# Performance work log

Hardware: AMD Instinct MI355X
Metric: run time of the kernel (lower is better)

## Reference

```python
import math
import jax, jax.numpy as jnp
import numpy as np
from jax import lax

jax.config.update("jax_enable_x64", True)

DECOMP_LEVEL = 5
# Daubechies-5 (db5) decomposition low-pass filter (pywt convention)
_DB5_LO = np.array([0.003335725285001549, -0.012580751999015526, -0.006241490213011705,
                    0.07757149384006515, -0.03224486958502952, -0.24229488706619015,
                    0.13842814590110342, 0.7243085284385744, 0.6038292697974729,
                    0.160102397974125], dtype=np.float64)
_L = _DB5_LO.size
_DB5_HI = _DB5_LO[::-1].copy() * ((-1.0) ** np.arange(_L))  # QMF high-pass
LO = jnp.asarray(_DB5_LO, jnp.float32)
HI = jnp.asarray(_DB5_HI, jnp.float32)
LOR = jnp.asarray(_DB5_LO[::-1].copy(), jnp.float32)
HIR = jnp.asarray(_DB5_HI[::-1].copy(), jnp.float32)


def _an_last(x):
    # orthonormal periodized analysis along last axis: (..., n) -> (..., n/2) x2
    n = x.shape[-1]
    lead = x.shape[:-1]
    xp = jnp.concatenate([x, x[..., : _L - 2]], axis=-1).reshape(-1, 1, n + _L - 2)
    k = jnp.stack([LO, HI])[:, None, :]  # (2,1,L)
    y = lax.conv_general_dilated(xp, k, (2,), "VALID")  # (B,2,n/2)
    y = y.reshape(lead + (2, n // 2))
    return y[..., 0, :], y[..., 1, :]


def _syn_last(a, d):
    # exact transpose/inverse of _an_last (orthonormal -> W^T = W^-1)
    n2 = a.shape[-1]
    n = 2 * n2
    lead = a.shape[:-1]
    B = int(np.prod(lead)) if lead else 1
    u = jnp.zeros((B, 2, n), a.dtype)
    u = u.at[:, 0, ::2].set(a.reshape(B, n2))
    u = u.at[:, 1, ::2].set(d.reshape(B, n2))
    up = jnp.concatenate([u[..., -(_L - 1):], u], axis=-1)  # circular left pad
    k = jnp.stack([LOR, HIR])[None, :, :]  # (1,2,L)
    y = lax.conv_general_dilated(up, k, (1,), "VALID")  # (B,1,n)
    return y.reshape(lead + (n,))


def _dwt2(x):  # x: (C,h,w) -> ll, lh, hl, hh each (C,h/2,w/2)
    a_h, d_h = _an_last(x.swapaxes(-1, -2))
    a_h = a_h.swapaxes(-1, -2)
    d_h = d_h.swapaxes(-1, -2)
    ll, lh = _an_last(a_h)
    hl, hh = _an_last(d_h)
    return ll, lh, hl, hh


def _idwt2(ll, lh, hl, hh):
    a_h = _syn_last(ll, lh)
    d_h = _syn_last(hl, hh)
    return _syn_last(a_h.swapaxes(-1, -2), d_h.swapaxes(-1, -2)).swapaxes(-1, -2)


def _estimate_noise(data):
    p = data.shape[0]
    rr = data @ data.T
    rri = jnp.linalg.inv(rr + 1e-6 * jnp.eye(p, dtype=data.dtype))
    def per_band(i):
        xx = rri - jnp.outer(rri[:, i], rri[i, :]) / rri[i, i]
        beta = xx @ rr[:, i]
        return beta.at[i].set(0.0)
    betas = jax.vmap(per_band)(jnp.arange(p))  # (p,p)
    return data - betas @ data


def hyres_forward(x):
    H, W, K = x.shape
    N = H * W
    data = x.reshape(N, K).T.astype(jnp.float64)
    w = _estimate_noise(data)
    omega1 = (jnp.sqrt(jnp.var(w, axis=1, ddof=1)) + 1e-30) ** 2  # (K,) f64
    y_w = x * omega1 ** -0.5  # whitened, f64
    u, s, v_pca = jnp.linalg.svd(y_w.reshape(N, K), full_matrices=False)
    pc = (u * s).reshape(W, H, K).astype(jnp.float32).transpose(2, 0, 1)  # (K,H,W)
    # multi-level 2D DWT per channel
    ll = pc
    highs = []
    for _ in range(DECOMP_LEVEL):
        ll, lh, hl, hh = _dwt2(ll)
        highs.append((lh, hl, hh))
    # overwrite-style full coefficient image [[LL,LH],[HL,HH]] recursively
    full = ll
    for lh, hl, hh in reversed(highs):
        top = jnp.concatenate([full, lh], axis=-1)
        bot = jnp.concatenate([hl, hh], axis=-1)
        full = jnp.concatenate([top, bot], axis=-2)
    V = full.transpose(1, 2, 0).reshape(N, K)
    V2 = V * V
    norm_v = jnp.sum(V2)
    n_xyz = jnp.asarray(V.size, jnp.float32)
    col_norm = jnp.sum(V2, axis=0)  # (K,)
    # SURE of soft-threshold over a 15-point grid in [0, sqrt(log N)]
    ts = np.linspace(0.0, math.sqrt(math.log(N)), 15).astype(np.float32)
    sure_cols = []
    for t in ts:
        t2 = float(t * t)
        s_t = (jnp.sum(jnp.minimum(V2, t2), axis=0)
               + 2.0 * jnp.sum((V2 > t2).astype(jnp.float32), axis=0)
               - col_norm)
        sure_cols.append(s_t)
    sure_all = jnp.stack(sure_cols, axis=1)  # (K,15)
    c_const = norm_v - n_xyz
    # replicate the in-place cumulative update: S_r = sum_{j<r} S_j + sure_r + C
    def step(acc, sure_r):
        s_r = acc + sure_r + c_const
        return acc + s_r, jnp.min(s_r)
    _, min_sure = lax.scan(step, jnp.zeros((15,), jnp.float32), sure_all)
    # early-exit: first rank>1 where min_sure increases; else loop ends at K-1
    cond = min_sure[2:] > min_sure[1:-1]
    rank = jnp.where(jnp.any(cond), 2 + jnp.argmax(cond), K - 1)
    mask = (jnp.arange(K) < rank).astype(jnp.float32)[:, None, None]
    # truncation-to-rank == zeroing channels >= rank (inverse DWT is linear)
    y = ll * mask
    for lh, hl, hh in reversed(highs):
        y = _idwt2(y, lh * mask, hl * mask, hh * mask)
    y_est = y.transpose(1, 2, 0).reshape(N, K)  # zero cols beyond rank
    out = (omega1.astype(jnp.float32) ** 0.5) * (y_est @ v_pca.astype(jnp.float32)).reshape(H, W, K)
    return out


def setup_inputs() -> dict:
    key = jax.random.key(0)
    k1, k2, k3 = jax.random.split(key, 3)
    H = W = 384
    K = 191
    R = 8  # low-rank spectral structure + noise, as HyRes assumes
    a = jax.random.normal(k1, (H * W, R), jnp.float32)
    b = jax.random.normal(k2, (R, K), jnp.float32)
    x = (a @ b) / np.sqrt(R) + 0.1 * jax.random.normal(k3, (H * W, K), jnp.float32)
    return {"x": x.reshape(H, W, K)}


def reference(x):
    return hyres_forward(x)
```

## Files before the change

### kernel.cpp

```cpp
#include <hip/hip_runtime.h>
#include <math.h>

#define K_     191
#define LD     192
#define N_     147456
#define MSUB   16
#define NT     15
#define TRI_N  18336
#define SMEM_SZ ((TRI_N + 192 + 192 + 1056) * 8)
#define SMEM2_SZ (6880 * 8 + 32 * 4 + TRI_N * 4)

#define NPAIR  6
#define NSPLIT 128
#define CHUNK  (N_ / NSPLIT)
#define RSTEP  32

__constant__ float c_lo[10] = {
  0.003335725285001549f, -0.012580751999015526f, -0.006241490213011705f,
  0.07757149384006515f,  -0.03224486958502952f, -0.24229488706619015f,
  0.13842814590110342f,   0.7243085284385744f,   0.6038292697974729f,
  0.160102397974125f };
__constant__ float c_hi[10] = {
  0.160102397974125f,    -0.6038292697974729f,   0.7243085284385744f,
 -0.13842814590110342f,  -0.24229488706619015f,  0.03224486958502952f,
  0.07757149384006515f,   0.006241490213011705f,-0.012580751999015526f,
 -0.003335725285001549f };

__global__ __launch_bounds__(256) void k_colsum(const float* __restrict__ x,
                                                double* __restrict__ m)
{
  int t = threadIdx.x;
  long base = (long)blockIdx.x * 512;
  if (t < K_) {
    double s = 0.0;
    const float* p = x + base * K_ + t;
    for (int r = 0; r < 512; ++r) s += (double)p[(long)r * K_];
    atomicAdd(&m[t], s);
  }
}

__global__ __launch_bounds__(256, 3) void k_rr(const float* __restrict__ x,
                                               double* __restrict__ rrg)
{
  __shared__ double Asd[RSTEP][64];
  __shared__ double Bsd[RSTEP][64];

  const int bid   = blockIdx.x;
  const int split = bid & (NSPLIT - 1);
  const int pair  = bid >> 7;
  const int BI[6] = {0, 0, 0, 1, 1, 2};
  const int BJ[6] = {0, 1, 2, 1, 2, 2};
  const int bi = BI[pair], bj = BJ[pair];
  const int ca = bi * 64, cb = bj * 64;

  const int t  = threadIdx.x;
  const int tx = t & 15, ty = t >> 4;
  const long n0 = (long)split * CHUNK;

  double acc[4][4];
  #pragma unroll
  for (int v = 0; v < 4; ++v)
    #pragma unroll
    for (int u = 0; u < 4; ++u) acc[v][u] = 0.0;

  for (int r0 = 0; r0 < CHUNK; r0 += RSTEP) {
    for (int s = t; s < RSTEP * 16; s += 256) {
      int row = s >> 4, g = s & 15;
      long gr = (n0 + r0 + row) * (long)K_;
      int c4a = ca + g * 4, c4b = cb + g * 4;
      #pragma unroll
      for (int e = 0; e < 4; ++e) {
        Asd[row][g * 4 + e] = (c4a + e < K_) ? (double)x[gr + c4a + e] : 0.0;
        Bsd[row][g * 4 + e] = (c4b + e < K_) ? (double)x[gr + c4b + e] : 0.0;
      }
    }
    __syncthreads();
    #pragma unroll 4
    for (int k = 0; k < RSTEP; ++k) {
      double a0 = Asd[k][ty],      a1 = Asd[k][ty + 16];
      double a2 = Asd[k][ty + 32], a3 = Asd[k][ty + 48];
      double b0 = Bsd[k][tx],      b1 = Bsd[k][tx + 16];
      double b2 = Bsd[k][tx + 32], b3 = Bsd[k][tx + 48];
      acc[0][0] += a0 * b0; acc[0][1] += a0 * b1; acc[0][2] += a0 * b2; acc[0][3] += a0 * b3;
      acc[1][0] += a1 * b0; acc[1][1] += a1 * b1; acc[1][2] += a1 * b2; acc[1][3] += a1 * b3;
      acc[2][0] += a2 * b0; acc[2][1] += a2 * b1; acc[2][2] += a2 * b2; acc[2][3] += a2 * b3;
      acc[3][0] += a3 * b0; acc[3][1] += a3 * b1; acc[3][2] += a3 * b2; acc[3][3] += a3 * b3;
    }
    __syncthreads();
  }

  #pragma unroll
  for (int v = 0; v < 4; ++v) {
    int mrow = ca + ty + 16 * v;
    #pragma unroll
    for (int u = 0; u < 4; ++u) {
      int ncol = cb + tx + 16 * u;
      if (mrow < K_ && ncol < K_)
        atomicAdd(&rrg[(size_t)mrow * K_ + ncol], acc[v][u]);
    }
  }
}

__global__ __launch_bounds__(256) void k_reduce(const double* __restrict__ rrg,
                                                double* __restrict__ rr)
{
  int idx = blockIdx.x * 256 + threadIdx.x;
  if (idx >= TRI_N) return;
  int i = (int)((sqrtf(8.f * (float)idx + 1.f) - 1.f) * 0.5f);
  while ((i + 1) * (i + 2) / 2 <= idx) ++i;
  while (i * (i + 1) / 2 > idx) --i;
  int j = idx - (i * (i + 1)) / 2;
  double s = rrg[(size_t)j * K_ + i];
  rr[i * LD + j] = s;
  rr[j * LD + i] = s;
}

__global__ __launch_bounds__(512) void k_small2(
    const double* __restrict__ rr, const double* __restrict__ m,
    double* __restrict__ invsq, float* __restrict__ sq32,
    float* __restrict__ normv)
{
  extern __shared__ double smem[];
  double* tri = smem;
  double* m_s = smem + TRI_N;
  double* w1  = m_s + 192;
  double* tmp = w1 + 192;
  const int t = threadIdx.x;

  if (t < K_) m_s[t] = m[t];
  for (int i = t >> 5; i < K_; i += 16) {
    int base = (i * (i + 1)) / 2;
    for (int j = t & 31; j <= i; j += 32) {
      double v = rr[i * LD + j];
      tri[base + j] = (i == j) ? v + 1e-6 : v;
    }
  }
  __syncthreads();

  for (int J = 0; J < 6; ++J) {
    const int j0 = J * 32;
    const int nb = (K_ - j0 < 32) ? (K_ - j0) : 32;

    if (t < 64) {
      const int rl = t & 31;
      double a[32];
      #pragma unroll
      for (int c = 0; c < 32; ++c) {
        int i = j0 + rl;
        a[c] = (c <= rl && rl < nb) ? tri[(i * (i + 1)) / 2 + j0 + c] : 0.0;
      }
      #pragma unroll
      for (int k = 0; k < 32; ++k) {
        double akk = __shfl(a[k], k);
        double piv = sqrt(akk);
        double inv = 1.0 / piv;
        if (t == k) tmp[k] = inv;
        a[k] = (rl == k) ? piv : a[k] * inv;
        #pragma unroll
        for (int c = k + 1; c < 32; ++c) {
          double lck = __shfl(a[k], c);
          if (c <= rl) a[c] -= a[k] * lck;
        }
      }
      if (t < 32 && rl < nb) {
        int i = j0 + rl;
        int rb = (i * (i + 1)) / 2 + j0;
        #pragma unroll
        for (int c = 0; c < 32; ++c)
          if (c <= rl) tri[rb + c] = a[c];
      }
    }
    __syncthreads();

    {
      int p = j0 + 32 + t;
      if (nb == 32 && p < K_) {
        int pb = (p * (p + 1)) / 2 + j0;
        double v[32];
        #pragma unroll
        for (int c = 0; c < 32; ++c) v[c] = tri[pb + c];
        #pragma unroll
        for (int c = 0; c < 32; ++c) {
          double s = v[c];
          #pragma unroll
          for (int q = 0; q < c; ++q) {
            int cc = j0 + c;
            s -= v[q] * tri[(cc * (cc + 1)) / 2 + j0 + q];
          }
          v[c] = s * tmp[c];
        }
        #pragma unroll
        for (int c = 0; c < 32; ++c) tri[pb + c] = v[c];
      }
    }
    __syncthreads();

    {
      int s0 = j0 + 32;
      int n = K_ - s0;
      if (n > 0) {
        int R4 = (n + 3) >> 2;
        int T4 = R4 * (R4 + 1) / 2;
        for (int tile = t; tile < T4; tile += 512) {
          int ti = (int)((sqrtf(8.f * (float)tile + 1.f) - 1.f) * 0.5f);
          while ((ti + 1) * (ti + 2) / 2 <= tile) ++ti;
          while (ti * (ti + 1) / 2 > tile) --ti;
          int tj = tile - ti * (ti + 1) / 2;
          int r0 = s0 + ti * 4, c0 = s0 + tj * 4;
          int rb[4], cb[4];
          #pragma unroll
          for (int u = 0; u < 4; ++u) {
            int r = (r0 + u < K_) ? r0 + u : K_ - 1;
            rb[u] = (r * (r + 1)) / 2;
            int c = (c0 + u < K_) ? c0 + u : K_ - 1;
            cb[u] = (c * (c + 1)) / 2;
          }
          double acc[4][4];
          #pragma unroll
          for (int u = 0; u < 4; ++u)
            #pragma unroll
            for (int v2 = 0; v2 < 4; ++v2) acc[u][v2] = 0.0;
          #pragma unroll 4
          for (int p = 0; p < 32; ++p) {
            double lr[4], lc[4];
            #pragma unroll
            for (int u = 0; u < 4; ++u) {
              lr[u] = tri[rb[u] + j0 + p];
              lc[u] = tri[cb[u] + j0 + p];
            }
            #pragma unroll
            for (int u = 0; u < 4; ++u)
              #pragma unroll
              for (int v2 = 0; v2 < 4; ++v2) acc[u][v2] += lr[u] * lc[v2];
          }
          #pragma unroll
          for (int u = 0; u < 4; ++u) {
            int r = r0 + u;
            if (r < K_) {
              #pragma unroll
              for (int v2 = 0; v2 < 4; ++v2) {
                int c = c0 + v2;
                if (c <= r) tri[rb[u] + c] -= acc[u][v2];
              }
            }
          }
        }
      }
    }
    __syncthreads();
  }

  for (int J = 0; J < 6; ++J) {
    const int j0 = J * 32;
    const int nb = (K_ - j0 < 32) ? (K_ - j0) : 32;
    if (t < 32) {
      int rd = (t < nb) ? j0 + t : K_ - 1;
      tmp[t] = 1.0 / tri[(rd * (rd + 1)) / 2 + rd];
    }
    __syncthreads();
    double xcol[32];
    if (t < 32) {
      const int c = t;
      #pragma unroll
      for (int r = 0; r < 32; ++r) {
        int rr_ = (j0 + r < K_) ? j0 + r : K_ - 1;
        int rb = (rr_ * (rr_ + 1)) / 2 + j0;
        double s = (r == c) ? 1.0 : 0.0;
        #pragma unroll
        for (int k = 0; k < 32; ++k)
          if (k < r) s -= tri[rb + k] * xcol[k];
        xcol[r] = s * tmp[r];
      }
    }
    __syncthreads();
    if (t < nb) {
      #pragma unroll
      for (int r = 0; r < 32; ++r) {
        int rr_ = j0 + r;
        if (r >= t && rr_ < K_)
          tri[(rr_ * (rr_ + 1)) / 2 + j0 + t] = xcol[r];
      }
    }
    __syncthreads();
  }

  for (int J = 0; J < 5; ++J) {
    const int j0 = J * 32;
    for (int idx = t; idx < 32 * 32; idx += 512) {
      int kk = idx >> 5, c = idx & 31;
      int row = j0 + kk;
      double v = 0.0;
      if (kk >= c && row < K_)
        v = tri[(row * (row + 1)) / 2 + j0 + c];
      tmp[kk * 33 + c] = v;
    }
    __syncthreads();
    for (int I = J + 1; I < 6; ++I) {
      const int i0 = I * 32;
      const int r = t & 31;
      #pragma unroll
      for (int half = 0; half < 2; ++half) {
        const int c = (t >> 5) + 16 * half;
        int ri = i0 + r;
        int ric = (ri < K_) ? ri : K_ - 1;
        int rb = (ric * (ric + 1)) / 2;
        double acc = 0.0;
        #pragma unroll
        for (int kk = 0; kk < 32; ++kk)
          acc += tri[rb + j0 + kk] * tmp[kk * 33 + c];
        for (int kb = j0 + 32; kb < i0; kb += 32) {
          #pragma unroll
          for (int kk = 0; kk < 32; ++kk) {
            int k = kb + kk;
            acc += tri[rb + k] * tri[(k * (k + 1)) / 2 + j0 + c];
          }
        }
        double out = 0.0;
        #pragma unroll
        for (int k = 0; k < 32; ++k) {
          double av = __shfl(acc, (t & 32) | k, 64);
          double xv = (k <= r) ? tri[rb + i0 + k] : 0.0;
          out -= xv * av;
        }
        if (ri < K_)
          tri[rb + j0 + c] = out;
      }
      __syncthreads();
    }
  }

  if (t < K_) {
    int r = t, rb = (r * (r + 1)) / 2;
    double s = 0.0;
    #pragma unroll 8
    for (int p = 0; p <= r; ++p) s += tri[rb + p] * m_s[p];
    w1[r] = s;
  }
  __syncthreads();
  if (t < K_) {
    int i = t;
    double s2 = 0.0, s1 = 0.0;
    #pragma unroll 8
    for (int r = i; r < K_; ++r) {
      double xv = tri[(r * (r + 1)) / 2 + i];
      s2 += xv * xv;
      s1 += xv * w1[r];
    }
    double dii = s2;
    double q = 1.0 / dii;
    double sm_ = s1 / dii;
    double var = (q - sm_ * sm_ / (double)N_) / (double)(N_ - 1);
    double t1 = sqrt(var) + 1e-30;
    double om = t1 * t1;
    invsq[i] = 1.0 / sqrt(om);
    sq32[i] = sqrtf((float)om);
    tmp[i] = rr[i * LD + i] / om;
  }
  __syncthreads();
  if (t < 64) {
    double s = 0.0;
    for (int i = t; i < K_; i += 64) s += tmp[i];
    #pragma unroll
    for (int off = 32; off > 0; off >>= 1) s += __shfl_down(s, off);
    if (t == 0) *normv = (float)s;
  }
}

__device__ __forceinline__ void cholqr(double* shQ, double* shS, int t)
{
  if (t < MSUB * MSUB) {
    int a = t & (MSUB - 1), b = t >> 4;
    double s = 0.0;
    for (int r = 0; r < K_; ++r) s += shQ[r * MSUB + a] * shQ[r * MSUB + b];
    shS[b * 17 + a] = s;
  }
  __syncthreads();
  for (int k = 0; k < MSUB; ++k) {
    if (t == 0) shS[k * 17 + k] = sqrt(shS[k * 17 + k]);
    __syncthreads();
    if (t > k && t < MSUB) shS[t * 17 + k] /= shS[k * 17 + k];
    __syncthreads();
    if (t < MSUB * MSUB) {
      int r = t & (MSUB - 1), c = t >> 4;
      if (c > k && r >= c) shS[r * 17 + c] -= shS[r * 17 + k] * shS[c * 17 + k];
    }
    __syncthreads();
  }
  if (t < K_) {
    double q[MSUB];
    #pragma unroll
    for (int c = 0; c < MSUB; ++c) {
      double v = shQ[t * MSUB + c];
      for (int p = 0; p < c; ++p) v -= q[p] * shS[c * 17 + p];
      q[c] = v / shS[c * 17 + c];
    }
    #pragma unroll
    for (int c = 0; c < MSUB; ++c) shQ[t * MSUB + c] = q[c];
  }
  __syncthreads();
}

__global__ __launch_bounds__(512) void k_sub(
    const double* __restrict__ rr, const double* __restrict__ invsq,
    float* __restrict__ W1, float* __restrict__ W2)
{
  extern __shared__ double dsm[];
  double* shQ  = dsm;
  double* shZ  = shQ + 3056;
  double* shS  = shZ + 3056;
  double* Ws   = shS + 272;
  double* inv_s= Ws + 272;
  double* ev   = inv_s + 192;
  double* cs_  = ev + 16;
  double* sn_  = cs_ + 8;
  int* ipp  = (int*)(sn_ + 8);
  int* iqq  = ipp + 8;
  int* perm = iqq + 8;
  float* tri = (float*)(perm + 16);
  const int t = threadIdx.x;

  if (t < K_) inv_s[t] = invsq[t];
  __syncthreads();
  for (int i = t >> 4; i < K_; i += 32) {
    int base = (i * (i + 1)) / 2;
    double di = inv_s[i];
    for (int j = t & 15; j <= i; j += 16)
      tri[base + j] = (float)(rr[i * LD + j] * di * inv_s[j]);
  }
  __syncthreads();

  for (int idx = t; idx < K_ * MSUB; idx += 512) {
    int i = idx >> 4, c = idx & 15;
    float g = (i >= c) ? tri[(i * (i + 1)) / 2 + c] : tri[(c * (c + 1)) / 2 + i];
    shQ[idx] = (double)g;
  }
  __syncthreads();

  cholqr(shQ, shS, t);
  for (int it = 0; it < 4; ++it) {
    for (int idx = t; idx < K_ * MSUB; idx += 512) shZ[idx] = shQ[idx];
    __syncthreads();
    if (t < 96 * 4) {
      int i2 = t >> 2, c4 = t & 3;
      int r0 = 2 * i2, r1 = r0 + 1;
      int has1 = (r1 < K_);
      int rb0 = (r0 * (r0 + 1)) >> 1;
      int rb1 = has1 ? ((r1 * (r1 + 1)) >> 1) : rb0;
      int cb0 = c4 * 4;
      double s0a = 0.0, s0b = 0.0, s0c = 0.0, s0d = 0.0;
      double s1a = 0.0, s1b = 0.0, s1c = 0.0, s1d = 0.0;
      #pragma unroll 2
      for (int k = 0; k <= r0; ++k) {
        double g0 = (double)tri[rb0 + k];
        double g1 = (double)tri[rb1 + k];
        double za = shZ[k * MSUB + cb0],     zb = shZ[k * MSUB + cb0 + 1];
        double zc = shZ[k * MSUB + cb0 + 2], zd = shZ[k * MSUB + cb0 + 3];
        s0a += g0 * za; s0b += g0 * zb; s0c += g0 * zc; s0d += g0 * zd;
        s1a += g1 * za; s1b += g1 * zb; s1c += g1 * zc; s1d += g1 * zd;
      }
      if (has1) {
        double g0 = (double)tri[rb1 + r0];
        double g1 = (double)tri[rb1 + r1];
        double za = shZ[r1 * MSUB + cb0],     zb = shZ[r1 * MSUB + cb0 + 1];
        double zc = shZ[r1 * MSUB + cb0 + 2], zd = shZ[r1 * MSUB + cb0 + 3];
        s0a += g0 * za; s0b += g0 * zb; s0c += g0 * zc; s0d += g0 * zd;
        s1a += g1 * za; s1b += g1 * zb; s1c += g1 * zc; s1d += g1 * zd;
      }
      int kk = ((r1 + 1) * (r1 + 2)) >> 1;
      #pragma unroll 2
      for (int k = r1 + 1; k < K_; ++k) {
        double g0 = (double)tri[kk + r0];
        double g1 = (double)tri[kk + r1];
        double za = shZ[k * MSUB + cb0],     zb = shZ[k * MSUB + cb0 + 1];
        double zc = shZ[k * MSUB + cb0 + 2], zd = shZ[k * MSUB + cb0 + 3];
        s0a += g0 * za; s0b += g0 * zb; s0c += g0 * zc; s0d += g0 * zd;
        s1a += g1 * za; s1b += g1 * zb; s1c += g1 * zc; s1d += g1 * zd;
        kk += k + 1;
      }
      shQ[r0 * MSUB + cb0]     = s0a;
      shQ[r0 * MSUB + cb0 + 1] = s0b;
      shQ[r0 * MSUB + cb0 + 2] = s0c;
      shQ[r0 * MSUB + cb0 + 3] = s0d;
      if (has1) {
        shQ[r1 * MSUB + cb0]     = s1a;
        shQ[r1 * MSUB + cb0 + 1] = s1b;
        shQ[r1 * MSUB + cb0 + 2] = s1c;
        shQ[r1 * MSUB + cb0 + 3] = s1d;
      }
    }
    __syncthreads();
    if (it < 3) cholqr(shQ, shS, t);
  }
  if (t < MSUB * MSUB) {
    int a = t & 15, b = t >> 4;
    double s = 0.0;
    for (int r = 0; r < K_; ++r) s += shZ[r * MSUB + b] * shQ[r * MSUB + a];
    shS[b * 17 + a] = s;
  }
  if (t < MSUB * 17) Ws[t] = 0.0;
  __syncthreads();
  if (t < MSUB) Ws[t * 17 + t] = 1.0;
  __syncthreads();
  for (int sweep = 0; sweep < 6; ++sweep) {
    for (int round = 0; round < 15; ++round) {
      if (t < 8) {
        int ia = (t == 0) ? 0 : (1 + ((t - 1 + round) % 15));
        int ib = 1 + ((14 - t + round) % 15);
        int p = ia < ib ? ia : ib;
        int q = ia < ib ? ib : ia;
        double app = shS[p * 17 + p], aqq = shS[q * 17 + q], apq = shS[p * 17 + q];
        double c = 1.0, s = 0.0;
        if (fabs(apq) > 1e-30 * (fabs(app) + fabs(aqq)) && apq != 0.0) {
          double tau = (aqq - app) / (2.0 * apq);
          double tt = (tau >= 0.0 ? 1.0 : -1.0) / (fabs(tau) + sqrt(1.0 + tau * tau));
          c = 1.0 / sqrt(1.0 + tt * tt); s = tt * c;
        }
        cs_[t] = c; sn_[t] = s; ipp[t] = p; iqq[t] = q;
      }
      __syncthreads();
      if (t < 128) {
        int i = t & 15, mI = t >> 4;
        int p = ipp[mI], q = iqq[mI];
        double c = cs_[mI], s = sn_[mI];
        double u = shS[i * 17 + p], v = shS[i * 17 + q];
        shS[i * 17 + p] = c * u - s * v; shS[i * 17 + q] = s * u + c * v;
        double wu = Ws[i * 17 + p], wv = Ws[i * 17 + q];
        Ws[i * 17 + p] = c * wu - s * wv; Ws[i * 17 + q] = s * wu + c * wv;
      }
      __syncthreads();
      if (t < 128) {
        int j = t & 15, mI = t >> 4;
        int p = ipp[mI], q = iqq[mI];
        double c = cs_[mI], s = sn_[mI];
        double u = shS[p * 17 + j], v = shS[q * 17 + j];
        shS[p * 17 + j] = c * u - s * v; shS[q * 17 + j] = s * u + c * v;
      }
      __syncthreads();
    }
  }
  if (t == 0) {
    for (int i = 0; i < MSUB; ++i) { ev[i] = shS[i * 17 + i]; perm[i] = i; }
    for (int i = 0; i < MSUB; ++i) {
      int best = i;
      for (int j = i + 1; j < MSUB; ++j)
        if (ev[perm[j]] > ev[perm[best]]) best = j;
      int tp = perm[i]; perm[i] = perm[best]; perm[best] = tp;
    }
  }
  __syncthreads();
  for (int idx = t; idx < K_ * MSUB; idx += 512) {
    int i = idx >> 4, c = idx & 15;
    int pc_ = perm[c];
    double e = 0.0;
    #pragma unroll
    for (int p = 0; p < MSUB; ++p) e += shZ[i * MSUB + p] * Ws[p * 17 + pc_];
    W1[i * MSUB + c] = (float)(inv_s[i] * e);
    W2[c * K_ + i]   = (float)(e / inv_s[i]);
  }
}

__global__ __launch_bounds__(256) void k_pc(const float* __restrict__ x,
                                            const float* __restrict__ W1,
                                            float* __restrict__ pc)
{
  __shared__ float xs[32][192];
  __shared__ float w1s[K_ * MSUB];
  int t = threadIdx.x;
  long n0 = (long)blockIdx.x * 32;
  for (int idx = t; idx < K_ * MSUB; idx += 256) w1s[idx] = W1[idx];
  for (int idx = t; idx < 32 * K_; idx += 256) {
    int row = idx / K_, col = idx - row * K_;
    xs[row][col] = x[(n0 + row) * K_ + col];
  }
  __syncthreads();
  int c = t & 15, nl = t >> 4;
  float a0 = 0.f, a1 = 0.f;
  for (int k = 0; k < K_; ++k) {
    float w = w1s[k * MSUB + c];
    a0 += xs[nl][k] * w;
    a1 += xs[nl + 16][k] * w;
  }
  __syncthreads();
  float* ts = &xs[0][0];
  ts[c * 33 + nl]      = a0;
  ts[c * 33 + nl + 16] = a1;
  __syncthreads();
  for (int idx = t; idx < MSUB * 32; idx += 256) {
    int cc = idx >> 5, nn = idx & 31;
    pc[(size_t)cc * N_ + n0 + nn] = ts[cc * 33 + nn];
  }
}

__global__ __launch_bounds__(256) void k_dwtv(const float* __restrict__ in,
                                              float* __restrict__ outv, int s)
{
  long gid = (long)blockIdx.x * 256 + threadIdx.x;
  int h = s >> 1;
  long per = (long)h * s;
  if (gid >= MSUB * per) return;
  int ch = (int)(gid / per);
  long rem = gid - (long)ch * per;
  int r = (int)(rem / s);
  int col = (int)(rem - (long)r * s);
  const float* cin = in + (long)ch * s * s;
  float la = 0.f, ld_ = 0.f;
  int base = 2 * r;
  #pragma unroll
  for (int l = 0; l < 10; ++l) {
    int rr_ = base + l; if (rr_ >= s) rr_ -= s;
    float v = cin[(long)rr_ * s + col];
    la += c_lo[l] * v; ld_ += c_hi[l] * v;
  }
  float* cout = outv + (long)ch * s * s;
  cout[(long)r * s + col] = la;
  cout[(long)(h + r) * s + col] = ld_;
}

__global__ __launch_bounds__(256) void k_dwth(const float* __restrict__ inv,
                                              float* __restrict__ llout,
                                              float* __restrict__ coef,
                                              int s, long offL, int last)
{
  long gid = (long)blockIdx.x * 256 + threadIdx.x;
  int h = s >> 1;
  long per = (long)s * h;
  if (gid >= MSUB * per) return;
  int ch = (int)(gid / per);
  long rem = gid - (long)ch * per;
  int r = (int)(rem / h);
  int mcol = (int)(rem - (long)r * h);
  const float* row = inv + (long)ch * s * s + (long)r * s;
  float lo = 0.f, hi = 0.f;
  int base = 2 * mcol;
  #pragma unroll
  for (int l = 0; l < 10; ++l) {
    int cc = base + l; if (cc >= s) cc -= s;
    float v = row[cc];
    lo += c_lo[l] * v; hi += c_hi[l] * v;
  }
  float* cslab = coef + (size_t)ch * N_ + offL;
  if (r < h) {
    llout[(size_t)ch * h * h + (long)r * h + mcol] = lo;
    if (last) coef[(size_t)ch * N_ + 147312 + (long)r * h + mcol] = lo;
    cslab[(long)r * h + mcol] = hi;
  } else {
    int rd = r - h;
    cslab[(long)h * h + (long)rd * h + mcol] = lo;
    cslab[(long)2 * h * h + (long)rd * h + mcol] = hi;
  }
}

__global__ __launch_bounds__(256) void k_stats(const float* __restrict__ coef,
                                               float* __restrict__ stats)
{
  int ch = blockIdx.x;
  int t = threadIdx.x;
  float T2[NT];
  {
    double stop = sqrt(log(147456.0));
    double step = stop / 14.0;
    for (int i = 0; i < NT; ++i) {
      double td = (i == 14) ? stop : (double)i * step;
      float tf = (float)td;
      T2[i] = tf * tf;
    }
  }
  float cn = 0.f, sm[NT], ct[NT];
  #pragma unroll
  for (int i = 0; i < NT; ++i) { sm[i] = 0.f; ct[i] = 0.f; }
  const float* base = coef + (size_t)ch * N_;
  for (int idx = t; idx < N_; idx += 256) {
    float v = base[idx];
    float v2 = v * v;
    cn += v2;
    #pragma unroll
    for (int i = 0; i < NT; ++i) {
      sm[i] += fminf(v2, T2[i]);
      ct[i] += (v2 > T2[i]) ? 1.0f : 0.0f;
    }
  }
  __shared__ float red2[4][32];
  int lane = t & 63, wv = t >> 6;
  for (int a = 0; a < 31; ++a) {
    float val = (a == 0) ? cn : ((a < 16) ? sm[a - 1] : ct[a - 16]);
    #pragma unroll
    for (int off = 32; off > 0; off >>= 1) val += __shfl_down(val, off);
    if (lane == 0) red2[wv][a] = val;
  }
  __syncthreads();
  if (t < 31)
    stats[ch * 31 + t] = red2[0][t] + red2[1][t] + red2[2][t] + red2[3][t];
}

__global__ void k_rank(const float* __restrict__ stats,
                       const float* __restrict__ normv, int* __restrict__ rankp)
{
  if (threadIdx.x != 0 || blockIdx.x != 0) return;
  float c_const = *normv - 28164096.0f;
  float acc[NT];
  for (int i = 0; i < NT; ++i) acc[i] = 0.f;
  float minsure[MSUB];
  for (int r = 0; r < MSUB; ++r) {
    float cn = stats[r * 31 + 0];
    float mn = 3.4e38f;
    for (int i = 0; i < NT; ++i) {
      float sure = stats[r * 31 + 1 + i] + 2.0f * stats[r * 31 + 16 + i] - cn;
      float s_r = acc[i] + sure + c_const;
      acc[i] = acc[i] + s_r;
      if (s_r < mn) mn = s_r;
    }
    minsure[r] = mn;
  }
  int rank = -1;
  for (int r = 2; r < MSUB; ++r) {
    if (minsure[r] > minsure[r - 1]) { rank = r; break; }
  }
  if (rank < 0) rank = MSUB - 1;
  *rankp = rank;
}

__global__ __launch_bounds__(256) void k_out(const float* __restrict__ pc,
                                             const float* __restrict__ W2,
                                             const int* __restrict__ rankp,
                                             float* __restrict__ out)
{
  long gid = (long)blockIdx.x * 256 + threadIdx.x;
  int n = (int)(gid / K_);
  int j = (int)(gid - (long)n * K_);
  int rank = *rankp;
  float acc = 0.f;
  for (int c = 0; c < rank; ++c)
    acc += pc[(size_t)c * N_ + n] * W2[c * K_ + j];
  out[gid] = acc;
}

extern "C" void kernel_launch(void* const* d_in, const int* in_sizes, int n_in,
                              void* d_out, int out_size, void* d_ws, size_t ws_size,
                              hipStream_t stream)
{
  if (n_in < 1 || in_sizes[0] != N_ * K_) return;
  const float* x = (const float*)d_in[0];
  float* out = (float*)d_out;
  (void)out_size;

  char* w = (char*)d_ws;
  size_t off = 0;
  auto alloc = [&](size_t bytes) -> char* {
    char* p = w + off;
    off = (off + bytes + 255) & ~(size_t)255;
    return p;
  };
  double* m_    = (double*)alloc(K_ * 8);
  double* rrp   = (double*)alloc((size_t)K_ * K_ * 8);
  double* rr    = (double*)alloc((size_t)K_ * LD * 8);
  double* invsq = (double*)alloc(K_ * 8);
  float*  sq32  = (float*)alloc(K_ * 4);
  float*  normv = (float*)alloc(256);
  float*  W1    = (float*)alloc((size_t)K_ * MSUB * 4);
  float*  W2    = (float*)alloc((size_t)MSUB * K_ * 4);
  float*  pc    = (float*)alloc((size_t)MSUB * N_ * 4);
  float*  tmpv  = (float*)alloc((size_t)MSUB * N_ * 4);
  float*  coef  = (float*)alloc((size_t)MSUB * N_ * 4);
  float*  curA  = (float*)alloc((size_t)MSUB * 192 * 192 * 4);
  float*  curB  = (float*)alloc((size_t)MSUB * 96 * 96 * 4);
  float*  stats = (float*)alloc((size_t)MSUB * 31 * 4);
  int*    rankp = (int*)alloc(256);
  if (off > ws_size) return;

  hipMemsetAsync(m_, 0, K_ * sizeof(double), stream);
  hipMemsetAsync(rrp, 0, (size_t)K_ * K_ * sizeof(double), stream);

  hipFuncSetAttribute(reinterpret_cast<const void*>(k_small2),
                      hipFuncAttributeMaxDynamicSharedMemorySize, SMEM_SZ);
  hipFuncSetAttribute(reinterpret_cast<const void*>(k_sub),
                      hipFuncAttributeMaxDynamicSharedMemorySize, SMEM2_SZ);

  k_colsum<<<N_ / 512, 256, 0, stream>>>(x, m_);
  k_rr<<<NPAIR * NSPLIT, 256, 0, stream>>>(x, rrp);
  k_reduce<<<(TRI_N + 255) / 256, 256, 0, stream>>>(rrp, rr);
  k_small2<<<1, 512, SMEM_SZ, stream>>>(rr, m_, invsq, sq32, normv);
  k_sub<<<1, 512, SMEM2_SZ, stream>>>(rr, invsq, W1, W2);
  k_pc<<<N_ / 32, 256, 0, stream>>>(x, W1, pc);

  int   sizes[5] = {384, 192, 96, 48, 24};
  long  offs[5]  = {0, 110592, 138240, 145152, 146880};
  float* lls[5]  = {curA, curB, curA, curB, curA};
  const float* curin = pc;
  for (int lev = 0; lev < 5; ++lev) {
    int s = sizes[lev], h = s >> 1;
    long nth = (long)MSUB * h * s;
    k_dwtv<<<(int)((nth + 255) / 256), 256, 0, stream>>>(curin, tmpv, s);
    k_dwth<<<(int)((nth + 255) / 256), 256, 0, stream>>>(tmpv, lls[lev], coef,
                                                         s, offs[lev],
                                                         lev == 4 ? 1 : 0);
    curin = lls[lev];
  }

  k_stats<<<MSUB, 256, 0, stream>>>(coef, stats);
  k_rank<<<1, 64, 0, stream>>>(stats, normv, rankp);
  k_out<<<(N_ * K_) / 256, 256, 0, stream>>>(pc, W2, rankp, out);
}
```

Before: 1.646 ms.

## Split single-block Cholesky inverse into multi-block column solves

The single-block kernel that did the Cholesky, the triangular inverse and the noise statistics is split into three kernels. The Cholesky stays on one block and writes L and its reciprocal diagonal to global memory. A new kernel with 192 blocks then does per-column forward substitution to get the inverse-diagonal norms, plus one block that solves for R^-1 m, replacing the serial blocked in-place triangular inversion. This spreads the serial solve across many CUs at the cost of two extra launches and a global round trip of L, and each solve is still a sequential loop over rows.

After: 1.476 ms. -10.3%, faster.

```diff
diff --git a/kernel.cpp b/kernel.cpp
--- a/kernel.cpp
+++ b/kernel.cpp
@@ -7,7 +7,8 @@
 #define MSUB   16
 #define NT     15
 #define TRI_N  18336
-#define SMEM_SZ ((TRI_N + 192 + 192 + 1056) * 8)
+#define SMEM_CHOL  ((TRI_N + 1056) * 8)
+#define SMEM_SOLVE ((TRI_N + 192 + 192 + 192) * 8)
 #define SMEM2_SZ (6880 * 8 + 32 * 4 + TRI_N * 4)
 
 #define NPAIR  6
@@ -115,19 +116,15 @@
   rr[j * LD + i] = s;
 }
 
-__global__ __launch_bounds__(512) void k_small2(
-    const double* __restrict__ rr, const double* __restrict__ m,
-    double* __restrict__ invsq, float* __restrict__ sq32,
-    float* __restrict__ normv)
+__global__ __launch_bounds__(512) void k_chol(
+    const double* __restrict__ rr, double* __restrict__ Lg,
+    double* __restrict__ rdg)
 {
   extern __shared__ double smem[];
   double* tri = smem;
-  double* m_s = smem + TRI_N;
-  double* w1  = m_s + 192;
-  double* tmp = w1 + 192;
+  double* tmp = smem + TRI_N;
   const int t = threadIdx.x;
 
-  if (t < K_) m_s[t] = m[t];
   for (int i = t >> 5; i < K_; i += 16) {
     int base = (i * (i + 1)) / 2;
     for (int j = t & 31; j <= i; j += 32) {
@@ -154,7 +151,10 @@
         double akk = __shfl(a[k], k);
         double piv = sqrt(akk);
         double inv = 1.0 / piv;
-        if (t == k) tmp[k] = inv;
+        if (t == k) {
+          tmp[k] = inv;
+          if (j0 + k < K_) rdg[j0 + k] = inv;
+        }
         a[k] = (rl == k) ? piv : a[k] * inv;
         #pragma unroll
         for (int c = k + 1; c < 32; ++c) {
@@ -250,116 +250,114 @@
     __syncthreads();
   }
 
-  for (int J = 0; J < 6; ++J) {
-    const int j0 = J * 32;
-    const int nb = (K_ - j0 < 32) ? (K_ - j0) : 32;
-    if (t < 32) {
-      int rd = (t < nb) ? j0 + t : K_ - 1;
-      tmp[t] = 1.0 / tri[(rd * (rd + 1)) / 2 + rd];
-    }
-    __syncthreads();
-    double xcol[32];
-    if (t < 32) {
-      const int c = t;
+  for (int idx = t; idx < TRI_N; idx += 512) Lg[idx] = tri[idx];
+}
+
+__global__ __launch_bounds__(256) void k_csolve(
+    const double* __restrict__ Lg, const double* __restrict__ rdg,
+    const double* __restrict__ mg, double* __restrict__ s2g,
+    double* __restrict__ zg)
+{
+  extern __shared__ double ssm[];
+  double* Ls   = ssm;
+  double* rd_s = Ls + TRI_N;
+  double* m_sh = rd_s + 192;
+  double* ys   = m_sh + 192;
+  const int t = threadIdx.x;
+  const int bid = blockIdx.x;
+
+  const int start = (bid < K_) ? (bid * (bid + 1)) / 2 : 0;
+  for (int idx = start + t; idx < TRI_N; idx += 256) Ls[idx] = Lg[idx];
+  if (t < K_) { rd_s[t] = rdg[t]; m_sh[t] = mg[t]; }
+  __syncthreads();
+
+  if (t >= 64) return;
+  const int l = t;
+
+  if (bid < K_) {
+    const int i = bid;
+    double x0 = 0.0, x1 = 0.0, x2 = 0.0;
+    {
+      double rdi = rd_s[i];
+      if ((i & 63) == l) {
+        int sl = i >> 6;
+        if (sl == 0) x0 = rdi; else if (sl == 1) x1 = rdi; else x2 = rdi;
+      }
+    }
+    for (int r = i + 1; r < K_; ++r) {
+      int rb = (r * (r + 1)) >> 1;
+      double partial = 0.0;
+      { int k = l;       if (k < r) partial += Ls[rb + k] * x0; }
+      { int k = l + 64;  if (k < r) partial += Ls[rb + k] * x1; }
+      { int k = l + 128; if (k < r) partial += Ls[rb + k] * x2; }
       #pragma unroll
-      for (int r = 0; r < 32; ++r) {
-        int rr_ = (j0 + r < K_) ? j0 + r : K_ - 1;
-        int rb = (rr_ * (rr_ + 1)) / 2 + j0;
-        double s = (r == c) ? 1.0 : 0.0;
-        #pragma unroll
-        for (int k = 0; k < 32; ++k)
-          if (k < r) s -= tri[rb + k] * xcol[k];
-        xcol[r] = s * tmp[r];
-      }
-    }
-    __syncthreads();
-    if (t < nb) {
+      for (int mm = 32; mm > 0; mm >>= 1) partial += __shfl_xor(partial, mm);
+      double val = -partial * rd_s[r];
+      if ((r & 63) == l) {
+        int sl = r >> 6;
+        if (sl == 0) x0 = val; else if (sl == 1) x1 = val; else x2 = val;
+      }
+    }
+    double s2p = x0 * x0 + x1 * x1 + x2 * x2;
+    #pragma unroll
+    for (int mm = 32; mm > 0; mm >>= 1) s2p += __shfl_xor(s2p, mm);
+    if (l == 0) s2g[i] = s2p;
+  } else {
+    double y0 = 0.0, y1 = 0.0, y2 = 0.0;
+    for (int r = 0; r < K_; ++r) {
+      int rb = (r * (r + 1)) >> 1;
+      double partial = 0.0;
+      { int k = l;       if (k < r) partial += Ls[rb + k] * y0; }
+      { int k = l + 64;  if (k < r) partial += Ls[rb + k] * y1; }
+      { int k = l + 128; if (k < r) partial += Ls[rb + k] * y2; }
       #pragma unroll
-      for (int r = 0; r < 32; ++r) {
-        int rr_ = j0 + r;
-        if (r >= t && rr_ < K_)
-          tri[(rr_ * (rr_ + 1)) / 2 + j0 + t] = xcol[r];
-      }
-    }
-    __syncthreads();
-  }
-
-  for (int J = 0; J < 5; ++J) {
-    const int j0 = J * 32;
-    for (int idx = t; idx < 32 * 32; idx += 512) {
-      int kk = idx >> 5, c = idx & 31;
-      int row = j0 + kk;
-      double v = 0.0;
-      if (kk >= c && row < K_)
-        v = tri[(row * (row + 1)) / 2 + j0 + c];
-      tmp[kk * 33 + c] = v;
-    }
-    __syncthreads();
-    for (int I = J + 1; I < 6; ++I) {
-      const int i0 = I * 32;
-      const int r = t & 31;
+      for (int mm = 32; mm > 0; mm >>= 1) partial += __shfl_xor(partial, mm);
+      double val = (m_sh[r] - partial) * rd_s[r];
+      if ((r & 63) == l) {
+        int sl = r >> 6;
+        if (sl == 0) y0 = val; else if (sl == 1) y1 = val; else y2 = val;
+      }
+      if (l == 0) ys[r] = val;
+    }
+    double z0 = 0.0, z1 = 0.0, z2 = 0.0;
+    for (int r = K_ - 1; r >= 0; --r) {
+      double partial = 0.0;
+      { int k = l;       if (k > r && k < K_) partial += Ls[((k * (k + 1)) >> 1) + r] * z0; }
+      { int k = l + 64;  if (k > r && k < K_) partial += Ls[((k * (k + 1)) >> 1) + r] * z1; }
+      { int k = l + 128; if (k > r && k < K_) partial += Ls[((k * (k + 1)) >> 1) + r] * z2; }
       #pragma unroll
-      for (int half = 0; half < 2; ++half) {
-        const int c = (t >> 5) + 16 * half;
-        int ri = i0 + r;
-        int ric = (ri < K_) ? ri : K_ - 1;
-        int rb = (ric * (ric + 1)) / 2;
-        double acc = 0.0;
-        #pragma unroll
-        for (int kk = 0; kk < 32; ++kk)
-          acc += tri[rb + j0 + kk] * tmp[kk * 33 + c];
-        for (int kb = j0 + 32; kb < i0; kb += 32) {
-          #pragma unroll
-          for (int kk = 0; kk < 32; ++kk) {
-            int k = kb + kk;
-            acc += tri[rb + k] * tri[(k * (k + 1)) / 2 + j0 + c];
-          }
-        }
-        double out = 0.0;
-        #pragma unroll
-        for (int k = 0; k < 32; ++k) {
-          double av = __shfl(acc, (t & 32) | k, 64);
-          double xv = (k <= r) ? tri[rb + i0 + k] : 0.0;
-          out -= xv * av;
-        }
-        if (ri < K_)
-          tri[rb + j0 + c] = out;
-      }
-      __syncthreads();
-    }
-  }
-
+      for (int mm = 32; mm > 0; mm >>= 1) partial += __shfl_xor(partial, mm);
+      double val = (ys[r] - partial) * rd_s[r];
+      if ((r & 63) == l) {
+        int sl = r >> 6;
+        if (sl == 0) z0 = val; else if (sl == 1) z1 = val; else z2 = val;
+      }
+      if (l == 0) zg[r] = val;
+    }
+  }
+}
+
+__global__ __launch_bounds__(256) void k_finals(
+    const double* __restrict__ rr, const double* __restrict__ s2g,
+    const double* __restrict__ zg, double* __restrict__ invsq,
+    float* __restrict__ normv)
+{
+  __shared__ double tmps[K_];
+  const int t = threadIdx.x;
   if (t < K_) {
-    int r = t, rb = (r * (r + 1)) / 2;
-    double s = 0.0;
-    #pragma unroll 8
-    for (int p = 0; p <= r; ++p) s += tri[rb + p] * m_s[p];
-    w1[r] = s;
-  }
-  __syncthreads();
-  if (t < K_) {
-    int i = t;
-    double s2 = 0.0, s1 = 0.0;
-    #pragma unroll 8
-    for (int r = i; r < K_; ++r) {
-      double xv = tri[(r * (r + 1)) / 2 + i];
-      s2 += xv * xv;
-      s1 += xv * w1[r];
-    }
-    double dii = s2;
+    double dii = s2g[t];
     double q = 1.0 / dii;
-    double sm_ = s1 / dii;
+    double sm_ = zg[t] / dii;
     double var = (q - sm_ * sm_ / (double)N_) / (double)(N_ - 1);
     double t1 = sqrt(var) + 1e-30;
     double om = t1 * t1;
-    invsq[i] = 1.0 / sqrt(om);
-    sq32[i] = sqrtf((float)om);
-    tmp[i] = rr[i * LD + i] / om;
+    invsq[t] = 1.0 / sqrt(om);
+    tmps[t] = rr[t * LD + t] / om;
   }
   __syncthreads();
   if (t < 64) {
     double s = 0.0;
-    for (int i = t; i < K_; i += 64) s += tmp[i];
+    for (int i = t; i < K_; i += 64) s += tmps[i];
     #pragma unroll
     for (int off = 32; off > 0; off >>= 1) s += __shfl_down(s, off);
     if (t == 0) *normv = (float)s;
@@ -753,8 +751,11 @@
   double* m_    = (double*)alloc(K_ * 8);
   double* rrp   = (double*)alloc((size_t)K_ * K_ * 8);
   double* rr    = (double*)alloc((size_t)K_ * LD * 8);
+  double* Lg    = (double*)alloc((size_t)TRI_N * 8);
+  double* rdg   = (double*)alloc(192 * 8);
+  double* s2g   = (double*)alloc(192 * 8);
+  double* zg    = (double*)alloc(192 * 8);
   double* invsq = (double*)alloc(K_ * 8);
-  float*  sq32  = (float*)alloc(K_ * 4);
   float*  normv = (float*)alloc(256);
   float*  W1    = (float*)alloc((size_t)K_ * MSUB * 4);
   float*  W2    = (float*)alloc((size_t)MSUB * K_ * 4);
@@ -770,15 +771,19 @@
   hipMemsetAsync(m_, 0, K_ * sizeof(double), stream);
   hipMemsetAsync(rrp, 0, (size_t)K_ * K_ * sizeof(double), stream);
 
-  hipFuncSetAttribute(reinterpret_cast<const void*>(k_small2),
-                      hipFuncAttributeMaxDynamicSharedMemorySize, SMEM_SZ);
+  hipFuncSetAttribute(reinterpret_cast<const void*>(k_chol),
+                      hipFuncAttributeMaxDynamicSharedMemorySize, SMEM_CHOL);
+  hipFuncSetAttribute(reinterpret_cast<const void*>(k_csolve),
+                      hipFuncAttributeMaxDynamicSharedMemorySize, SMEM_SOLVE);
   hipFuncSetAttribute(reinterpret_cast<const void*>(k_sub),
                       hipFuncAttributeMaxDynamicSharedMemorySize, SMEM2_SZ);
 
   k_colsum<<<N_ / 512, 256, 0, stream>>>(x, m_);
   k_rr<<<NPAIR * NSPLIT, 256, 0, stream>>>(x, rrp);
   k_reduce<<<(TRI_N + 255) / 256, 256, 0, stream>>>(rrp, rr);
-  k_small2<<<1, 512, SMEM_SZ, stream>>>(rr, m_, invsq, sq32, normv);
+  k_chol<<<1, 512, SMEM_CHOL, stream>>>(rr, Lg, rdg);
+  k_csolve<<<K_ + 1, 256, SMEM_SOLVE, stream>>>(Lg, rdg, m_, s2g, zg);
+  k_finals<<<1, 256, 0, stream>>>(rr, s2g, zg, invsq, normv);
   k_sub<<<1, 512, SMEM2_SZ, stream>>>(rr, invsq, W1, W2);
   k_pc<<<N_ / 32, 256, 0, stream>>>(x, W1, pc);
 
```
